# Optimization experiments

Measured on AMD Instinct MI355X. Metric: run time of the kernel, lower is better.

The kernel has to match this reference:

```python
import jax, jax.numpy as jnp
import numpy as np

DIM = 256
HEADS = 8
WS = 7          # window_size
WN = 8          # window_num per side
H = W = WS * WN # 56
B = 32
MLP_HIDDEN = 4 * DIM
SCALE = (DIM // HEADS) ** -0.5
LN_EPS = 1e-5


def _rel_index(ws):
    # pairwise relative position index inside a ws x ws window (dense 0..(2ws-1)^2-1,
    # so remap_position_index is the identity relabeling)
    ch, cw = np.meshgrid(np.arange(ws), np.arange(ws), indexing='ij')
    cf = np.stack([ch.ravel(), cw.ravel()])            # (2, ws*ws)
    rel = cf[:, :, None] - cf[:, None, :]              # (2, N, N)
    rel = rel.transpose(1, 2, 0).astype(np.int32)
    rel[..., 0] += ws - 1
    rel[..., 1] += ws - 1
    rel[..., 0] *= 2 * ws - 1
    return rel.sum(-1)                                 # (N, N) in [0, (2ws-1)^2)


def _layernorm(x, g, b):
    m = x.mean(-1, keepdims=True)
    v = ((x - m) ** 2).mean(-1, keepdims=True)
    return (x - m) * jax.lax.rsqrt(v + LN_EPS) * g + b


def _mhsa(x, qkv_w, qkv_b, proj_w, proj_b, bias):
    # x: (B_, N, C); bias: (nH, N, N) or None
    B_, N, C = x.shape
    hd = C // HEADS
    qkv = (x @ qkv_w.T + qkv_b).reshape(B_, N, 3, HEADS, hd).transpose(2, 0, 3, 1, 4)
    q, k, v = qkv[0], qkv[1], qkv[2]
    attn = jnp.einsum('bhqd,bhkd->bhqk', q * SCALE, k)
    if bias is not None:
        attn = attn + bias[None]
    attn = jax.nn.softmax(attn, axis=-1)
    out = jnp.einsum('bhqk,bhkd->bhqd', attn, v).transpose(0, 2, 1, 3).reshape(B_, N, C)
    return out @ proj_w.T + proj_b


def setup_inputs() -> dict:
    key = jax.random.key(0)
    ks = jax.random.split(key, 8)
    f32 = jnp.float32
    return {
        'regional_tokens': jax.random.normal(ks[0], (B, WN * WN, DIM), f32),
        'x': jax.random.normal(ks[1], (B, H * W, DIM), f32),
        'norm1_g': jnp.ones((DIM,), f32), 'norm1_b': jnp.zeros((DIM,), f32),
        'norm2_g': jnp.ones((DIM,), f32), 'norm2_b': jnp.zeros((DIM,), f32),
        'norm3_g': jnp.ones((DIM,), f32), 'norm3_b': jnp.zeros((DIM,), f32),
        'qkv_w': jax.random.normal(ks[2], (3 * DIM, DIM), f32) * 0.02,
        'qkv_b': jnp.zeros((3 * DIM,), f32),
        'proj_w': jax.random.normal(ks[3], (DIM, DIM), f32) * 0.02,
        'proj_b': jnp.zeros((DIM,), f32),
        'bias_table': jax.random.normal(ks[4], ((2 * WS - 1) ** 2, HEADS), f32) * 0.02,
        'fc1_w': jax.random.normal(ks[5], (MLP_HIDDEN, DIM), f32) * 0.02,
        'fc1_b': jnp.zeros((MLP_HIDDEN,), f32),
        'fc2_w': jax.random.normal(ks[6], (DIM, MLP_HIDDEN), f32) * 0.02,
        'fc2_b': jnp.zeros((DIM,), f32),
        'rel_index': jnp.asarray(_rel_index(WS)),
    }


def reference(regional_tokens, x, norm1_g, norm1_b, norm2_g, norm2_b, norm3_g, norm3_b,
              qkv_w, qkv_b, proj_w, proj_b, bias_table, fc1_w, fc1_b, fc2_w, fc2_b,
              rel_index):
    Bb, L, C = x.shape
    nW = regional_tokens.shape[1]
    ws2 = WS * WS
    # --- RSA: attention over regional tokens (no relative bias) ---
    regional_tokens = regional_tokens + _mhsa(
        _layernorm(regional_tokens, norm1_g, norm1_b), qkv_w, qkv_b, proj_w, proj_b, None)
    # --- window partition of x: (B,H,W,C) -> (nW*B, ws*ws, C) (batch-major) ---
    xw = x.reshape(Bb, H // WS, WS, W // WS, WS, C)
    xw = xw.transpose(0, 1, 3, 2, 4, 5).reshape(-1, ws2, C)
    # regional tokens reshaped window-major, exactly as the torch code does
    reg = regional_tokens.transpose(1, 0, 2).reshape(nW * Bb, 1, C)
    t = jnp.concatenate([reg, xw], axis=1)  # (nW*B, 1+ws2, C)
    # --- LSA relative position bias, zero-padded for the regional token ---
    bias = bias_table[rel_index]                       # (ws2, ws2, nH)
    bias = jnp.pad(bias, ((1, 0), (1, 0), (0, 0)))      # (1+ws2, 1+ws2, nH)
    bias = bias.transpose(2, 0, 1)                      # (nH, N, N)
    t = t + _mhsa(_layernorm(t, norm2_g, norm2_b), qkv_w, qkv_b, proj_w, proj_b, bias)
    # --- MLP ---
    h = _layernorm(t, norm3_g, norm3_b)
    h = jax.nn.gelu(h @ fc1_w.T + fc1_b, approximate=False) @ fc2_w.T + fc2_b
    t = t + h
    # --- split back ---
    reg_out = t[:, 0, :].reshape(nW, Bb, C).transpose(1, 0, 2)   # (B, nW, C)
    xw = t[:, 1:, :].reshape(Bb, H // WS, W // WS, WS, WS, C)
    x_out = xw.transpose(0, 1, 3, 2, 4, 5).reshape(Bb, L, C)
    return reg_out, x_out
```

## Files before the change

### kernel.cpp

```cpp
#include <hip/hip_runtime.h>
#include <math.h>

#define SCALE_Q 0.17677669529663687f

typedef __attribute__((ext_vector_type(8))) short bf16x8;
typedef __attribute__((ext_vector_type(4))) float f32x4;
typedef __attribute__((ext_vector_type(4))) unsigned short u16x4;

static __device__ __forceinline__ unsigned short f2bf(float f) {
    unsigned int u = __float_as_uint(f);
    u += 0x7FFF + ((u >> 16) & 1);
    return (unsigned short)(u >> 16);
}

__global__ void prep_kernel(const float* __restrict__ qkv_w, const float* __restrict__ proj_w,
                            const float* __restrict__ fc1_w, const float* __restrict__ fc2_w,
                            const float* __restrict__ bias_table, const int* __restrict__ rel_index,
                            unsigned short* __restrict__ wq, unsigned short* __restrict__ wp,
                            unsigned short* __restrict__ w1, unsigned short* __restrict__ w2,
                            float* __restrict__ bias_pad) {
    int tid = blockIdx.x * blockDim.x + threadIdx.x;
    int stride = gridDim.x * blockDim.x;
    for (int i = tid; i < 768 * 256; i += stride) wq[i] = f2bf(qkv_w[i]);
    for (int i = tid; i < 256 * 256; i += stride) wp[i] = f2bf(proj_w[i]);
    for (int i = tid; i < 1024 * 256; i += stride) w1[i] = f2bf(fc1_w[i]);
    for (int i = tid; i < 256 * 1024; i += stride) w2[i] = f2bf(fc2_w[i]);
    for (int i = tid; i < 8 * 64 * 64; i += stride) {
        int h = i >> 12, q = (i >> 6) & 63, k = i & 63;
        float v;
        if (k >= 50) v = -1e30f;
        else if (q == 0 || k == 0 || q >= 50) v = 0.f;
        else v = bias_table[rel_index[(q - 1) * 49 + (k - 1)] * 8 + h];
        bias_pad[i] = v;
    }
}

template <int IS_RSA>
__global__ __launch_bounds__(1024, 4) void attn_kernel(
    const float* __restrict__ reg_tok, const float* __restrict__ x,
    const float* __restrict__ reg2_in, float* __restrict__ out,
    const float* __restrict__ ln_g, const float* __restrict__ ln_b,
    const unsigned short* __restrict__ wq, const float* __restrict__ qkv_b,
    const unsigned short* __restrict__ wp, const float* __restrict__ proj_b,
    const float* __restrict__ bias_pad) {
    __shared__ __align__(16) unsigned char smem[147456];
    unsigned short* regA = (unsigned short*)smem;
    unsigned short* regB = (unsigned short*)(smem + 36864);
    unsigned short* vT   = (unsigned short*)(smem + 110592);

    const int tid = threadIdx.x;
    const int lane = tid & 63;
    const int wid = tid >> 6;
    const int l15 = lane & 15;
    const int lg = lane >> 4;
    const int u = blockIdx.x;
    const int NV = IS_RSA ? 64 : 50;
    const f32x4 fzero = {0.f, 0.f, 0.f, 0.f};

    int reg_off = 0, xb = 0, wi = 0, wj = 0;
    if (!IS_RSA) {
        reg_off = ((u & 31) * 64 + (u >> 5)) * 256;
        xb = u >> 6;
        int xn = u & 63;
        wi = xn >> 3; wj = xn & 7;
    }

    for (int r = wid; r < 64; r += 16) {
        if (r < NV) {
            const float* src;
            if (IS_RSA) src = reg_tok + (u * 64 + r) * 256;
            else if (r == 0) src = reg2_in + reg_off;
            else {
                int p = r - 1;
                src = x + (xb * 3136 + (wi * 7 + p / 7) * 56 + (wj * 7 + p % 7)) * 256;
            }
            f32x4 v = *(const f32x4*)(src + lane * 4);
            float s = v[0] + v[1] + v[2] + v[3];
            float s2 = v[0] * v[0] + v[1] * v[1] + v[2] * v[2] + v[3] * v[3];
            #pragma unroll
            for (int m = 1; m < 64; m <<= 1) { s += __shfl_xor(s, m); s2 += __shfl_xor(s2, m); }
            float mean = s * 0.00390625f;
            float rstd = rsqrtf(s2 * 0.00390625f - mean * mean + 1e-5f);
            u16x4 o;
            #pragma unroll
            for (int j = 0; j < 4; ++j) {
                int c = lane * 4 + j;
                o[j] = f2bf((v[j] - mean) * rstd * ln_g[c] + ln_b[c]);
            }
            *(u16x4*)(regA + r * 264 + lane * 4) = o;
        } else {
            u16x4 z = {0, 0, 0, 0};
            *(u16x4*)(regA + r * 264 + lane * 4) = z;
        }
    }
    __syncthreads();

    {
        f32x4 acc[4][3];
        #pragma unroll
        for (int mi = 0; mi < 4; ++mi)
            #pragma unroll
            for (int t = 0; t < 3; ++t) acc[mi][t] = fzero;
        #pragma unroll
        for (int ks = 0; ks < 8; ++ks) {
            int k = ks * 32 + lg * 8;
            bf16x8 a[4], b[3];
            #pragma unroll
            for (int mi = 0; mi < 4; ++mi) a[mi] = *(const bf16x8*)(regA + (mi * 16 + l15) * 264 + k);
            #pragma unroll
            for (int t = 0; t < 3; ++t) b[t] = *(const bf16x8*)(wq + (wid * 48 + t * 16 + l15) * 256 + k);
            #pragma unroll
            for (int mi = 0; mi < 4; ++mi)
                #pragma unroll
                for (int t = 0; t < 3; ++t)
                    acc[mi][t] = __builtin_amdgcn_mfma_f32_16x16x32_bf16(a[mi], b[t], acc[mi][t], 0, 0, 0);
        }
        #pragma unroll
        for (int mi = 0; mi < 4; ++mi)
            #pragma unroll
            for (int t = 0; t < 3; ++t) {
                int col = wid * 48 + t * 16 + l15;
                float bias = qkv_b[col];
                #pragma unroll
                for (int r = 0; r < 4; ++r) {
                    int row = mi * 16 + lg * 4 + r;
                    unsigned short hv = f2bf(acc[mi][t][r] + bias);
                    if (col < 512) regB[row * 520 + col] = hv;
                    else vT[(col - 512) * 72 + row] = hv;
                }
            }
    }
    __syncthreads();

    const int h = wid >> 1;
    const int sub = wid & 1;
    const int qb = sub * 32;
    f32x4 s[2][4];
    {
        int k0 = h * 32 + lg * 8;
        bf16x8 a[2], b[4];
        #pragma unroll
        for (int mi = 0; mi < 2; ++mi) a[mi] = *(const bf16x8*)(regB + (qb + mi * 16 + l15) * 520 + k0);
        #pragma unroll
        for (int ni = 0; ni < 4; ++ni) b[ni] = *(const bf16x8*)(regB + (ni * 16 + l15) * 520 + 256 + k0);
        #pragma unroll
        for (int mi = 0; mi < 2; ++mi)
            #pragma unroll
            for (int ni = 0; ni < 4; ++ni)
                s[mi][ni] = __builtin_amdgcn_mfma_f32_16x16x32_bf16(a[mi], b[ni], fzero, 0, 0, 0);
    }
    #pragma unroll
    for (int mi = 0; mi < 2; ++mi) {
        #pragma unroll
        for (int r = 0; r < 4; ++r) {
            int row_g = qb + mi * 16 + lg * 4 + r;
            float sv[4];
            #pragma unroll
            for (int ni = 0; ni < 4; ++ni) {
                float t = s[mi][ni][r] * SCALE_Q;
                if (!IS_RSA) t += bias_pad[h * 4096 + row_g * 64 + ni * 16 + l15];
                sv[ni] = t;
            }
            float mx = fmaxf(fmaxf(sv[0], sv[1]), fmaxf(sv[2], sv[3]));
            mx = fmaxf(mx, __shfl_xor(mx, 1));
            mx = fmaxf(mx, __shfl_xor(mx, 2));
            mx = fmaxf(mx, __shfl_xor(mx, 4));
            mx = fmaxf(mx, __shfl_xor(mx, 8));
            float sum = 0.f;
            #pragma unroll
            for (int ni = 0; ni < 4; ++ni) { sv[ni] = __expf(sv[ni] - mx); sum += sv[ni]; }
            sum += __shfl_xor(sum, 1);
            sum += __shfl_xor(sum, 2);
            sum += __shfl_xor(sum, 4);
            sum += __shfl_xor(sum, 8);
            float inv = 1.f / sum;
            #pragma unroll
            for (int ni = 0; ni < 4; ++ni) s[mi][ni][r] = sv[ni] * inv;
        }
    }
    __syncthreads();

    unsigned short* P = regB + wid * 2304;
    #pragma unroll
    for (int mi = 0; mi < 2; ++mi)
        #pragma unroll
        for (int ni = 0; ni < 4; ++ni)
            #pragma unroll
            for (int r = 0; r < 4; ++r)
                P[(mi * 16 + lg * 4 + r) * 72 + ni * 16 + l15] = f2bf(s[mi][ni][r]);

    f32x4 ov[2][2];
    #pragma unroll
    for (int mi = 0; mi < 2; ++mi) { ov[mi][0] = fzero; ov[mi][1] = fzero; }
    #pragma unroll
    for (int kc = 0; kc < 2; ++kc) {
        int k = kc * 32 + lg * 8;
        bf16x8 a[2], b[2];
        #pragma unroll
        for (int mi = 0; mi < 2; ++mi) a[mi] = *(const bf16x8*)(P + (mi * 16 + l15) * 72 + k);
        #pragma unroll
        for (int n2 = 0; n2 < 2; ++n2) b[n2] = *(const bf16x8*)(vT + (h * 32 + n2 * 16 + l15) * 72 + k);
        #pragma unroll
        for (int mi = 0; mi < 2; ++mi)
            #pragma unroll
            for (int n2 = 0; n2 < 2; ++n2)
                ov[mi][n2] = __builtin_amdgcn_mfma_f32_16x16x32_bf16(a[mi], b[n2], ov[mi][n2], 0, 0, 0);
    }
    #pragma unroll
    for (int mi = 0; mi < 2; ++mi)
        #pragma unroll
        for (int n2 = 0; n2 < 2; ++n2)
            #pragma unroll
            for (int r = 0; r < 4; ++r)
                regA[(qb + mi * 16 + lg * 4 + r) * 264 + h * 32 + n2 * 16 + l15] = f2bf(ov[mi][n2][r]);
    __syncthreads();

    {
        int nb = wid * 16;
        f32x4 acc[4];
        #pragma unroll
        for (int mi = 0; mi < 4; ++mi) acc[mi] = fzero;
        #pragma unroll
        for (int ks = 0; ks < 8; ++ks) {
            int k = ks * 32 + lg * 8;
            bf16x8 a[4], b;
            #pragma unroll
            for (int mi = 0; mi < 4; ++mi) a[mi] = *(const bf16x8*)(regA + (mi * 16 + l15) * 264 + k);
            b = *(const bf16x8*)(wp + (nb + l15) * 256 + k);
            #pragma unroll
            for (int mi = 0; mi < 4; ++mi)
                acc[mi] = __builtin_amdgcn_mfma_f32_16x16x32_bf16(a[mi], b, acc[mi], 0, 0, 0);
        }
        int col = nb + l15;
        float pb = proj_b[col];
        #pragma unroll
        for (int mi = 0; mi < 4; ++mi)
            #pragma unroll
            for (int r = 0; r < 4; ++r) {
                int row = mi * 16 + lg * 4 + r;
                if (row < NV) {
                    float val = acc[mi][r] + pb;
                    if (IS_RSA) {
                        int off = (u * 64 + row) * 256 + col;
                        out[off] = val + reg_tok[off];
                    } else if (row == 0) {
                        out[reg_off + col] = val + reg2_in[reg_off + col];
                    } else {
                        int p = row - 1;
                        int off = (xb * 3136 + (wi * 7 + p / 7) * 56 + (wj * 7 + p % 7)) * 256 + col;
                        out[524288 + off] = val + x[off];
                    }
                }
            }
    }
}

__global__ __launch_bounds__(512, 4) void mlp_kernel(
    float* __restrict__ dout,
    const float* __restrict__ ln_g, const float* __restrict__ ln_b,
    const unsigned short* __restrict__ w1, const float* __restrict__ b1,
    const unsigned short* __restrict__ w2, const float* __restrict__ b2) {
    __shared__ __align__(16) unsigned short xln[64 * 264];
    __shared__ __align__(16) unsigned short hld[64 * 264];
    const int tid = threadIdx.x;
    const int lane = tid & 63;
    const int wid = tid >> 6;
    const int l15 = lane & 15;
    const int lg = lane >> 4;
    const int u = blockIdx.x;
    const f32x4 fzero = {0.f, 0.f, 0.f, 0.f};

    int reg_off = ((u & 31) * 64 + (u >> 5)) * 256;
    int xb = u >> 6;
    int xn = u & 63;
    int wi = xn >> 3, wj = xn & 7;
    float* xsec = dout + 524288;

    for (int r = wid; r < 64; r += 8) {
        if (r < 50) {
            const float* src = (r == 0)
                ? (dout + reg_off)
                : (xsec + (xb * 3136 + (wi * 7 + (r - 1) / 7) * 56 + (wj * 7 + (r - 1) % 7)) * 256);
            f32x4 v = *(const f32x4*)(src + lane * 4);
            float s = v[0] + v[1] + v[2] + v[3];
            float s2 = v[0] * v[0] + v[1] * v[1] + v[2] * v[2] + v[3] * v[3];
            #pragma unroll
            for (int m = 1; m < 64; m <<= 1) { s += __shfl_xor(s, m); s2 += __shfl_xor(s2, m); }
            float mean = s * 0.00390625f;
            float rstd = rsqrtf(s2 * 0.00390625f - mean * mean + 1e-5f);
            u16x4 o;
            #pragma unroll
            for (int j = 0; j < 4; ++j) {
                int c = lane * 4 + j;
                o[j] = f2bf((v[j] - mean) * rstd * ln_g[c] + ln_b[c]);
            }
            *(u16x4*)(xln + r * 264 + lane * 4) = o;
        } else {
            u16x4 z = {0, 0, 0, 0};
            *(u16x4*)(xln + r * 264 + lane * 4) = z;
        }
    }
    __syncthreads();

    f32x4 acc2[4][2];
    #pragma unroll
    for (int mi = 0; mi < 4; ++mi) { acc2[mi][0] = fzero; acc2[mi][1] = fzero; }

    for (int c = 0; c < 4; ++c) {
        f32x4 acc1[4][2];
        #pragma unroll
        for (int mi = 0; mi < 4; ++mi) { acc1[mi][0] = fzero; acc1[mi][1] = fzero; }
        int hb = c * 256 + wid * 32;
        #pragma unroll
        for (int ks = 0; ks < 8; ++ks) {
            int k = ks * 32 + lg * 8;
            bf16x8 a[4], b[2];
            #pragma unroll
            for (int mi = 0; mi < 4; ++mi) a[mi] = *(const bf16x8*)(xln + (mi * 16 + l15) * 264 + k);
            #pragma unroll
            for (int ni = 0; ni < 2; ++ni) b[ni] = *(const bf16x8*)(w1 + (hb + ni * 16 + l15) * 256 + k);
            #pragma unroll
            for (int mi = 0; mi < 4; ++mi)
                #pragma unroll
                for (int ni = 0; ni < 2; ++ni)
                    acc1[mi][ni] = __builtin_amdgcn_mfma_f32_16x16x32_bf16(a[mi], b[ni], acc1[mi][ni], 0, 0, 0);
        }
        #pragma unroll
        for (int mi = 0; mi < 4; ++mi)
            #pragma unroll
            for (int ni = 0; ni < 2; ++ni) {
                int hc = wid * 32 + ni * 16 + l15;
                float bb = b1[c * 256 + hc];
                #pragma unroll
                for (int r = 0; r < 4; ++r) {
                    int row = mi * 16 + lg * 4 + r;
                    float v = acc1[mi][ni][r] + bb;
                    float g = 0.5f * v * (1.f + erff(v * 0.70710678118654752f));
                    hld[row * 264 + hc] = f2bf(g);
                }
            }
        __syncthreads();
        #pragma unroll
        for (int ks = 0; ks < 8; ++ks) {
            int k = ks * 32 + lg * 8;
            bf16x8 a[4], b[2];
            #pragma unroll
            for (int mi = 0; mi < 4; ++mi) a[mi] = *(const bf16x8*)(hld + (mi * 16 + l15) * 264 + k);
            #pragma unroll
            for (int ni = 0; ni < 2; ++ni)
                b[ni] = *(const bf16x8*)(w2 + (wid * 32 + ni * 16 + l15) * 1024 + c * 256 + k);
            #pragma unroll
            for (int mi = 0; mi < 4; ++mi)
                #pragma unroll
                for (int ni = 0; ni < 2; ++ni)
                    acc2[mi][ni] = __builtin_amdgcn_mfma_f32_16x16x32_bf16(a[mi], b[ni], acc2[mi][ni], 0, 0, 0);
        }
        __syncthreads();
    }
    #pragma unroll
    for (int mi = 0; mi < 4; ++mi)
        #pragma unroll
        for (int ni = 0; ni < 2; ++ni) {
            int col = wid * 32 + ni * 16 + l15;
            float bb = b2[col];
            #pragma unroll
            for (int r = 0; r < 4; ++r) {
                int row = mi * 16 + lg * 4 + r;
                if (row < 50) {
                    float* dst = (row == 0)
                        ? (dout + reg_off + col)
                        : (xsec + (xb * 3136 + (wi * 7 + (row - 1) / 7) * 56 + (wj * 7 + (row - 1) % 7)) * 256 + col);
                    *dst = acc2[mi][ni][r] + bb + *dst;
                }
            }
        }
}

extern "C" void kernel_launch(void* const* d_in, const int* in_sizes, int n_in,
                              void* d_out, int out_size, void* d_ws, size_t ws_size,
                              hipStream_t stream) {
    const float* regional = (const float*)d_in[0];
    const float* x = (const float*)d_in[1];
    const float* n1g = (const float*)d_in[2];
    const float* n1b = (const float*)d_in[3];
    const float* n2g = (const float*)d_in[4];
    const float* n2b = (const float*)d_in[5];
    const float* n3g = (const float*)d_in[6];
    const float* n3b = (const float*)d_in[7];
    const float* qkvw = (const float*)d_in[8];
    const float* qkvb = (const float*)d_in[9];
    const float* projw = (const float*)d_in[10];
    const float* projb = (const float*)d_in[11];
    const float* btab = (const float*)d_in[12];
    const float* f1w = (const float*)d_in[13];
    const float* f1b = (const float*)d_in[14];
    const float* f2w = (const float*)d_in[15];
    const float* f2b = (const float*)d_in[16];
    const int* relidx = (const int*)d_in[17];

    unsigned char* ws = (unsigned char*)d_ws;
    unsigned short* wq = (unsigned short*)(ws);
    unsigned short* wp = (unsigned short*)(ws + 393216);
    unsigned short* w1 = (unsigned short*)(ws + 524288);
    unsigned short* w2 = (unsigned short*)(ws + 1048576);
    float* bias_pad    = (float*)(ws + 1572864);
    float* reg2        = (float*)(ws + 1703936);

    float* out = (float*)d_out;

    prep_kernel<<<512, 256, 0, stream>>>(qkvw, projw, f1w, f2w, btab, relidx, wq, wp, w1, w2, bias_pad);
    attn_kernel<1><<<32, 1024, 0, stream>>>(regional, x, nullptr, reg2, n1g, n1b, wq, qkvb, wp, projb, nullptr);
    attn_kernel<0><<<2048, 1024, 0, stream>>>(regional, x, reg2, out, n2g, n2b, wq, qkvb, wp, projb, bias_pad);
    mlp_kernel<<<2048, 512, 0, stream>>>(out, n3g, n3b, w1, f1b, w2, f2b);
}
```

Before: 558.8 us.

## Keep attention probabilities in registers via transposed S and use tanh-GELU

Computes the score tile transposed (K as A operand, Q as B) so each lane holds a column of probabilities that can be fed straight into the PV MFMA as register operands. This removes the LDS round trip for P and one block barrier, shrinks shared memory, and hoists the relative-position bias loads into vector loads before the barrier. The V x P MFMA pads each operand half with zeros, so half of every MFMA does no useful work. Separately, exact erf GELU is replaced by a tanh/sigmoid approximation with a fast reciprocal, which changes numerics slightly.

```diff
diff --git a/kernel.cpp b/kernel.cpp
--- a/kernel.cpp
+++ b/kernel.cpp
@@ -11,6 +11,12 @@
     unsigned int u = __float_as_uint(f);
     u += 0x7FFF + ((u >> 16) & 1);
     return (unsigned short)(u >> 16);
+}
+
+static __device__ __forceinline__ float gelu_fast(float v) {
+    float s = v * (0.7978845608f + 0.0356774081f * v * v);
+    float e = __expf(-2.0f * s);
+    return v * __builtin_amdgcn_rcpf(1.0f + e);
 }
 
 __global__ void prep_kernel(const float* __restrict__ qkv_w, const float* __restrict__ proj_w,
@@ -43,10 +49,10 @@
     const unsigned short* __restrict__ wq, const float* __restrict__ qkv_b,
     const unsigned short* __restrict__ wp, const float* __restrict__ proj_b,
     const float* __restrict__ bias_pad) {
-    __shared__ __align__(16) unsigned char smem[147456];
+    __shared__ __align__(16) unsigned char smem[140288];
     unsigned short* regA = (unsigned short*)smem;
     unsigned short* regB = (unsigned short*)(smem + 36864);
-    unsigned short* vT   = (unsigned short*)(smem + 110592);
+    unsigned short* vT   = (unsigned short*)(smem + 103424);
 
     const int tid = threadIdx.x;
     const int lane = tid & 63;
@@ -94,6 +100,9 @@
         }
     }
     __syncthreads();
+
+    const int h = wid >> 1;
+    const int qb = (wid & 1) * 32;
 
     {
         f32x4 acc[4][3];
@@ -130,89 +139,99 @@
                 }
             }
     }
+
+    f32x4 bv[4][2];
+    if (!IS_RSA) {
+        #pragma unroll
+        for (int mi = 0; mi < 4; ++mi)
+            #pragma unroll
+            for (int nj = 0; nj < 2; ++nj)
+                bv[mi][nj] = *(const f32x4*)(bias_pad + h * 4096 + (qb + nj * 16 + l15) * 64 + mi * 16 + lg * 4);
+    }
     __syncthreads();
 
-    const int h = wid >> 1;
-    const int sub = wid & 1;
-    const int qb = sub * 32;
-    f32x4 s[2][4];
+    f32x4 st[4][2];
     {
         int k0 = h * 32 + lg * 8;
-        bf16x8 a[2], b[4];
-        #pragma unroll
-        for (int mi = 0; mi < 2; ++mi) a[mi] = *(const bf16x8*)(regB + (qb + mi * 16 + l15) * 520 + k0);
-        #pragma unroll
-        for (int ni = 0; ni < 4; ++ni) b[ni] = *(const bf16x8*)(regB + (ni * 16 + l15) * 520 + 256 + k0);
-        #pragma unroll
-        for (int mi = 0; mi < 2; ++mi)
-            #pragma unroll
-            for (int ni = 0; ni < 4; ++ni)
-                s[mi][ni] = __builtin_amdgcn_mfma_f32_16x16x32_bf16(a[mi], b[ni], fzero, 0, 0, 0);
-    }
-    #pragma unroll
-    for (int mi = 0; mi < 2; ++mi) {
-        #pragma unroll
-        for (int r = 0; r < 4; ++r) {
-            int row_g = qb + mi * 16 + lg * 4 + r;
-            float sv[4];
-            #pragma unroll
-            for (int ni = 0; ni < 4; ++ni) {
-                float t = s[mi][ni][r] * SCALE_Q;
-                if (!IS_RSA) t += bias_pad[h * 4096 + row_g * 64 + ni * 16 + l15];
-                sv[ni] = t;
-            }
-            float mx = fmaxf(fmaxf(sv[0], sv[1]), fmaxf(sv[2], sv[3]));
-            mx = fmaxf(mx, __shfl_xor(mx, 1));
-            mx = fmaxf(mx, __shfl_xor(mx, 2));
-            mx = fmaxf(mx, __shfl_xor(mx, 4));
-            mx = fmaxf(mx, __shfl_xor(mx, 8));
-            float sum = 0.f;
-            #pragma unroll
-            for (int ni = 0; ni < 4; ++ni) { sv[ni] = __expf(sv[ni] - mx); sum += sv[ni]; }
-            sum += __shfl_xor(sum, 1);
-            sum += __shfl_xor(sum, 2);
-            sum += __shfl_xor(sum, 4);
-            sum += __shfl_xor(sum, 8);
-            float inv = 1.f / sum;
-            #pragma unroll
-            for (int ni = 0; ni < 4; ++ni) s[mi][ni][r] = sv[ni] * inv;
-        }
-    }
-    __syncthreads();
-
-    unsigned short* P = regB + wid * 2304;
-    #pragma unroll
-    for (int mi = 0; mi < 2; ++mi)
-        #pragma unroll
-        for (int ni = 0; ni < 4; ++ni)
-            #pragma unroll
-            for (int r = 0; r < 4; ++r)
-                P[(mi * 16 + lg * 4 + r) * 72 + ni * 16 + l15] = f2bf(s[mi][ni][r]);
+        bf16x8 af[4], bfq[2];
+        #pragma unroll
+        for (int mi = 0; mi < 4; ++mi) af[mi] = *(const bf16x8*)(regB + (mi * 16 + l15) * 520 + 256 + k0);
+        #pragma unroll
+        for (int nj = 0; nj < 2; ++nj) bfq[nj] = *(const bf16x8*)(regB + (qb + nj * 16 + l15) * 520 + k0);
+        #pragma unroll
+        for (int mi = 0; mi < 4; ++mi)
+            #pragma unroll
+            for (int nj = 0; nj < 2; ++nj)
+                st[mi][nj] = __builtin_amdgcn_mfma_f32_16x16x32_bf16(af[mi], bfq[nj], fzero, 0, 0, 0);
+    }
+
+    u16x4 pf[4][2];
+    #pragma unroll
+    for (int nj = 0; nj < 2; ++nj) {
+        float ps[4][4];
+        float mx = -3.0e38f;
+        #pragma unroll
+        for (int mi = 0; mi < 4; ++mi)
+            #pragma unroll
+            for (int r = 0; r < 4; ++r) {
+                float t = st[mi][nj][r] * SCALE_Q;
+                if (!IS_RSA) t += bv[mi][nj][r];
+                ps[mi][r] = t;
+                mx = fmaxf(mx, t);
+            }
+        mx = fmaxf(mx, __shfl_xor(mx, 16));
+        mx = fmaxf(mx, __shfl_xor(mx, 32));
+        float sum = 0.f;
+        #pragma unroll
+        for (int mi = 0; mi < 4; ++mi)
+            #pragma unroll
+            for (int r = 0; r < 4; ++r) { ps[mi][r] = __expf(ps[mi][r] - mx); sum += ps[mi][r]; }
+        sum += __shfl_xor(sum, 16);
+        sum += __shfl_xor(sum, 32);
+        float inv = __builtin_amdgcn_rcpf(sum);
+        #pragma unroll
+        for (int mi = 0; mi < 4; ++mi) {
+            u16x4 p4;
+            #pragma unroll
+            for (int r = 0; r < 4; ++r) p4[r] = f2bf(ps[mi][r] * inv);
+            pf[mi][nj] = p4;
+        }
+    }
 
     f32x4 ov[2][2];
     #pragma unroll
-    for (int mi = 0; mi < 2; ++mi) { ov[mi][0] = fzero; ov[mi][1] = fzero; }
-    #pragma unroll
-    for (int kc = 0; kc < 2; ++kc) {
-        int k = kc * 32 + lg * 8;
-        bf16x8 a[2], b[2];
-        #pragma unroll
-        for (int mi = 0; mi < 2; ++mi) a[mi] = *(const bf16x8*)(P + (mi * 16 + l15) * 72 + k);
-        #pragma unroll
-        for (int n2 = 0; n2 < 2; ++n2) b[n2] = *(const bf16x8*)(vT + (h * 32 + n2 * 16 + l15) * 72 + k);
-        #pragma unroll
-        for (int mi = 0; mi < 2; ++mi)
-            #pragma unroll
-            for (int n2 = 0; n2 < 2; ++n2)
-                ov[mi][n2] = __builtin_amdgcn_mfma_f32_16x16x32_bf16(a[mi], b[n2], ov[mi][n2], 0, 0, 0);
-    }
-    #pragma unroll
-    for (int mi = 0; mi < 2; ++mi)
-        #pragma unroll
-        for (int n2 = 0; n2 < 2; ++n2)
-            #pragma unroll
-            for (int r = 0; r < 4; ++r)
-                regA[(qb + mi * 16 + lg * 4 + r) * 264 + h * 32 + n2 * 16 + l15] = f2bf(ov[mi][n2][r]);
+    for (int m2 = 0; m2 < 2; ++m2) { ov[m2][0] = fzero; ov[m2][1] = fzero; }
+    #pragma unroll
+    for (int kt = 0; kt < 4; ++kt) {
+        bf16x8 pb[2];
+        #pragma unroll
+        for (int nj = 0; nj < 2; ++nj) {
+            bf16x8 t;
+            t[0] = (short)pf[kt][nj][0]; t[1] = (short)pf[kt][nj][1];
+            t[2] = (short)pf[kt][nj][2]; t[3] = (short)pf[kt][nj][3];
+            t[4] = 0; t[5] = 0; t[6] = 0; t[7] = 0;
+            pb[nj] = t;
+        }
+        #pragma unroll
+        for (int m2 = 0; m2 < 2; ++m2) {
+            u16x4 av = *(const u16x4*)(vT + (h * 32 + m2 * 16 + l15) * 72 + kt * 16 + lg * 4);
+            bf16x8 a8;
+            a8[0] = (short)av[0]; a8[1] = (short)av[1]; a8[2] = (short)av[2]; a8[3] = (short)av[3];
+            a8[4] = 0; a8[5] = 0; a8[6] = 0; a8[7] = 0;
+            #pragma unroll
+            for (int nj = 0; nj < 2; ++nj)
+                ov[m2][nj] = __builtin_amdgcn_mfma_f32_16x16x32_bf16(a8, pb[nj], ov[m2][nj], 0, 0, 0);
+        }
+    }
+    #pragma unroll
+    for (int m2 = 0; m2 < 2; ++m2)
+        #pragma unroll
+        for (int nj = 0; nj < 2; ++nj) {
+            u16x4 o4;
+            #pragma unroll
+            for (int r = 0; r < 4; ++r) o4[r] = f2bf(ov[m2][nj][r]);
+            *(u16x4*)(regA + (qb + nj * 16 + l15) * 264 + h * 32 + m2 * 16 + lg * 4) = o4;
+        }
     __syncthreads();
 
     {
@@ -335,8 +354,7 @@
                 for (int r = 0; r < 4; ++r) {
                     int row = mi * 16 + lg * 4 + r;
                     float v = acc1[mi][ni][r] + bb;
-                    float g = 0.5f * v * (1.f + erff(v * 0.70710678118654752f));
-                    hld[row * 264 + hc] = f2bf(g);
+                    hld[row * 264 + hc] = f2bf(gelu_fast(v));
                 }
             }
         __syncthreads();
```

After: 541.8 us. -3.0%, faster.
